# Performance work log

Measured on AMD Instinct MI355X. Metric: run time of the kernel, lower is better.

The kernel has to match this reference:

```python
import jax, jax.numpy as jnp
import numpy as np

NUM_HEADS = 16
HEAD_SIZE = 64
D_MODEL = NUM_HEADS * HEAD_SIZE  # 1024


def setup_inputs() -> dict:
    key = jax.random.key(0)
    ks = jax.random.split(key, 12)
    B, S = 4, 2048
    q = jax.random.normal(ks[0], (B, S, D_MODEL), dtype=jnp.float32)
    k = jax.random.normal(ks[1], (B, S, D_MODEL), dtype=jnp.float32)
    v = jax.random.normal(ks[2], (B, S, D_MODEL), dtype=jnp.float32)
    w = jax.random.uniform(ks[3], (B, S), dtype=jnp.float32)
    scale = 1.0 / np.sqrt(D_MODEL)
    Wq = jax.random.normal(ks[4], (D_MODEL, D_MODEL), dtype=jnp.float32) * scale
    Wk = jax.random.normal(ks[5], (D_MODEL, D_MODEL), dtype=jnp.float32) * scale
    Wv = jax.random.normal(ks[6], (D_MODEL, D_MODEL), dtype=jnp.float32) * scale
    Wo = jax.random.normal(ks[7], (D_MODEL, D_MODEL), dtype=jnp.float32) * scale
    bq = jnp.zeros((D_MODEL,), jnp.float32)
    bk = jnp.zeros((D_MODEL,), jnp.float32)
    bv = jnp.zeros((D_MODEL,), jnp.float32)
    bo = jnp.zeros((D_MODEL,), jnp.float32)
    return {"q": q, "k": k, "v": v, "w": w,
            "Wq": Wq, "bq": bq, "Wk": Wk, "bk": bk,
            "Wv": Wv, "bv": bv, "Wo": Wo, "bo": bo}


def reference(q, k, v, w, Wq, bq, Wk, bk, Wv, bv, Wo, bo):
    B, S, _ = q.shape
    H, Dh = NUM_HEADS, HEAD_SIZE

    def split_heads(x):  # [B,S,D] -> [B,H,S,Dh]
        return x.reshape(B, -1, H, Dh).transpose(0, 2, 1, 3)

    q_h = split_heads(q @ Wq + bq)
    k_h = split_heads(k @ Wk + bk)
    v_h = split_heads(v @ Wv + bv)

    # [B,H,Sq,Sk]
    score = jnp.einsum('bhqd,bhkd->bhqk', q_h, k_h) / jnp.sqrt(
        jnp.asarray(Dh, jnp.float32))
    # weighted unnormalized softmax: exp(score)*w / sum (no max subtraction,
    # faithful to original)
    exp_score = jnp.exp(score) * w[:, None, None, :]
    attn = exp_score / (jnp.sum(exp_score, axis=-1, keepdims=True) + 1e-12)

    context = jnp.einsum('bhqk,bhkd->bhqd', attn, v_h)  # [B,H,S,Dh]
    context = context.transpose(0, 2, 1, 3).reshape(B, -1, H * Dh)
    return context @ Wo + bo
```

## Files before the change

### kernel.cpp

```cpp
#include <hip/hip_runtime.h>
#include <hip/hip_bf16.h>

typedef __bf16 bf16x8 __attribute__((ext_vector_type(8)));
typedef float f32x4 __attribute__((ext_vector_type(4)));
typedef float f32x16 __attribute__((ext_vector_type(16)));
typedef unsigned short u16;
typedef unsigned int u32;

#define SB 4
#define SS 2048
#define SD 1024
#define SH 16
#define SDH 64

__device__ __forceinline__ u16 f2bf(float f) {
  union { float f; u32 u; } x; x.f = f;
  u32 r = (x.u + 0x7FFFu + ((x.u >> 16) & 1u)) >> 16;
  return (u16)r;
}

__device__ __forceinline__ void gl_lds16(const void* g, void* l) {
  __builtin_amdgcn_global_load_lds(
      (__attribute__((address_space(1))) void*)g,
      (__attribute__((address_space(3))) void*)l, 16, 0, 0);
}

__global__ void log2w_kernel(const float* __restrict__ w,
                             float* __restrict__ lwg) {
  int i = blockIdx.x * 256 + threadIdx.x;
  lwg[i] = __builtin_amdgcn_logf(w[i]);
}

__global__ void transpose_cast_kernel(const float* __restrict__ W0,
                                      const float* __restrict__ W1,
                                      const float* __restrict__ W2,
                                      const float* __restrict__ W3,
                                      u16* __restrict__ T0,
                                      u16* __restrict__ T1,
                                      u16* __restrict__ T2,
                                      u16* __restrict__ T3) {
  __shared__ float t[32][33];
  int z = blockIdx.z;
  const float* W = (z == 0) ? W0 : (z == 1) ? W1 : (z == 2) ? W2 : W3;
  u16* Wt = (z == 0) ? T0 : (z == 1) ? T1 : (z == 2) ? T2 : T3;
  int bx = blockIdx.x, by = blockIdx.y;
  int tx = threadIdx.x, ty = threadIdx.y;
#pragma unroll
  for (int j = 0; j < 32; j += 8)
    t[ty + j][tx] = W[(size_t)(by * 32 + ty + j) * SD + bx * 32 + tx];
  __syncthreads();
#pragma unroll
  for (int j = 0; j < 32; j += 8)
    Wt[(size_t)(bx * 32 + ty + j) * SD + by * 32 + tx] = f2bf(t[tx][ty + j]);
}

template <int MODE>
__global__ __launch_bounds__(256, 2)
void gemm_bt(const void* __restrict__ Ap, const void* __restrict__ Btp,
             const float* __restrict__ bias, void* __restrict__ Out,
             int M, int N, int K) {
  constexpr bool CA = (MODE == 0 || MODE == 1);
  constexpr bool CB = (MODE == 2);
  __shared__ u16 Asl[2][128 * 64];
  __shared__ u16 Bsl[2][128 * 64];
  const u16* Ab = (const u16*)Ap;
  const float* Af = (const float*)Ap;
  const u16* Bb = (const u16*)Btp;
  const float* Bf = (const float*)Btp;

  const int ntile = N >> 7;
  int bid = blockIdx.x;
  bid = (bid & 7) * ((int)gridDim.x >> 3) + (bid >> 3);
  int m0 = (bid / ntile) * 128, n0 = (bid % ntile) * 128;
  int tid = threadIdx.x;
  int lane = tid & 63, wv = tid >> 6;
  int wr = wv >> 1, wc = wv & 1;

  float4 regA[4][2], regB[4][2];

  auto load_cast = [&](int k0) {
#pragma unroll
    for (int it = 0; it < 4; ++it) {
      int c = tid + it * 256;
      int row = c >> 3, sl = c & 7;
      if (CA) {
        const float* s = Af + (size_t)(m0 + row) * K + k0 + sl * 8;
        regA[it][0] = *(const float4*)s;
        regA[it][1] = *(const float4*)(s + 4);
      }
      if (CB) {
        const float* s = Bf + (size_t)(n0 + row) * K + k0 + sl * 8;
        regB[it][0] = *(const float4*)s;
        regB[it][1] = *(const float4*)(s + 4);
      }
    }
  };
  auto stage_lds = [&](int buf, int k0) {
#pragma unroll
    for (int it = 0; it < 4; ++it) {
      int c = tid + it * 256;
      int row = c >> 3, sl = c & 7;
      int ssl = sl ^ (row & 7);
      if (!CA)
        gl_lds16(Ab + (size_t)(m0 + row) * K + k0 + ssl * 8,
                 (char*)&Asl[buf][0] + c * 16);
      if (!CB)
        gl_lds16(Bb + (size_t)(n0 + row) * K + k0 + ssl * 8,
                 (char*)&Bsl[buf][0] + c * 16);
    }
  };
  auto write_cast = [&](int buf) {
#pragma unroll
    for (int it = 0; it < 4; ++it) {
      int c = tid + it * 256;
      int row = c >> 3, sl = c & 7;
      int dst = (row * 128 + sl * 16) ^ ((row & 7) << 4);
      if (CA) {
        uint4 o;
        asm("v_cvt_pk_bf16_f32 %0, %1, %2"
            : "=v"(o.x) : "v"(regA[it][0].x), "v"(regA[it][0].y));
        asm("v_cvt_pk_bf16_f32 %0, %1, %2"
            : "=v"(o.y) : "v"(regA[it][0].z), "v"(regA[it][0].w));
        asm("v_cvt_pk_bf16_f32 %0, %1, %2"
            : "=v"(o.z) : "v"(regA[it][1].x), "v"(regA[it][1].y));
        asm("v_cvt_pk_bf16_f32 %0, %1, %2"
            : "=v"(o.w) : "v"(regA[it][1].z), "v"(regA[it][1].w));
        *(uint4*)((char*)&Asl[buf][0] + dst) = o;
      }
      if (CB) {
        uint4 o;
        asm("v_cvt_pk_bf16_f32 %0, %1, %2"
            : "=v"(o.x) : "v"(regB[it][0].x), "v"(regB[it][0].y));
        asm("v_cvt_pk_bf16_f32 %0, %1, %2"
            : "=v"(o.y) : "v"(regB[it][0].z), "v"(regB[it][0].w));
        asm("v_cvt_pk_bf16_f32 %0, %1, %2"
            : "=v"(o.z) : "v"(regB[it][1].x), "v"(regB[it][1].y));
        asm("v_cvt_pk_bf16_f32 %0, %1, %2"
            : "=v"(o.w) : "v"(regB[it][1].z), "v"(regB[it][1].w));
        *(uint4*)((char*)&Bsl[buf][0] + dst) = o;
      }
    }
  };

  f32x4 acc[4][4] = {};
  load_cast(0);
  stage_lds(0, 0);
  write_cast(0);

  int nk = K >> 6;
  for (int kt = 0; kt < nk; ++kt) {
    int buf = kt & 1;
    if (kt + 1 < nk) {
      load_cast((kt + 1) << 6);
      stage_lds(buf ^ 1, (kt + 1) << 6);
      if (CA || CB)
        asm volatile("s_waitcnt vmcnt(12) lgkmcnt(0)" ::: "memory");
      else
        asm volatile("s_waitcnt vmcnt(8) lgkmcnt(0)" ::: "memory");
    } else {
      asm volatile("s_waitcnt vmcnt(0) lgkmcnt(0)" ::: "memory");
    }
    __builtin_amdgcn_s_barrier();
#pragma unroll
    for (int kk = 0; kk < 2; ++kk) {
      bf16x8 af[4], bfr[4];
#pragma unroll
      for (int i = 0; i < 4; ++i) {
        int ar = wr * 64 + i * 16 + (lane & 15);
        int abyt = (ar * 128 + (kk * 32 + (lane >> 4) * 8) * 2) ^
                   ((ar & 7) << 4);
        af[i] = *(const bf16x8*)((const char*)&Asl[buf][0] + abyt);
        int br = wc * 64 + i * 16 + (lane & 15);
        int bbyt = (br * 128 + (kk * 32 + (lane >> 4) * 8) * 2) ^
                   ((br & 7) << 4);
        bfr[i] = *(const bf16x8*)((const char*)&Bsl[buf][0] + bbyt);
      }
#pragma unroll
      for (int i = 0; i < 4; ++i)
#pragma unroll
        for (int j = 0; j < 4; ++j)
          acc[i][j] = __builtin_amdgcn_mfma_f32_16x16x32_bf16(
              af[i], bfr[j], acc[i][j], 0, 0, 0);
    }
    if (kt + 1 < nk) write_cast(buf ^ 1);
    __builtin_amdgcn_s_barrier();
  }

  int cg = lane >> 4, cc = lane & 15;
#pragma unroll
  for (int i = 0; i < 4; ++i) {
#pragma unroll
    for (int j = 0; j < 4; ++j) {
#pragma unroll
      for (int r = 0; r < 4; ++r) {
        int m = m0 + wr * 64 + i * 16 + cg * 4 + r;
        int n = n0 + wc * 64 + j * 16 + cc;
        float val = acc[i][j][r];
        if (MODE == 0) {
          val = (val + bias[n]) * 0.18033688011112042f;
          int b = m >> 11, s = m & 2047, h = n >> 6, dh = n & 63;
          ((u16*)Out)[((size_t)((b * SH + h) * SS + s) << 6) + dh] = f2bf(val);
        } else if (MODE == 1) {
          val += bias[n];
          int b = m >> 11, s = m & 2047, h = n >> 6, dh = n & 63;
          size_t off = ((size_t)(b * SH + h) << 17) + ((size_t)(s >> 5) << 11) +
                       ((size_t)(dh >> 4) << 9) +
                       ((size_t)((s & 31) | ((dh & 8) << 2)) << 3) + (dh & 7);
          ((u16*)Out)[off] = f2bf(val);
        } else if (MODE == 2) {
          val += bias[m];
          int h = m >> 6, dh = m & 63, b = n >> 11, s = n & 2047;
          size_t off = ((size_t)(b * SH + h) << 17) + ((size_t)(s >> 4) << 10) +
                       ((size_t)(dh >> 5) << 9) +
                       ((size_t)(((s >> 3) & 1) * 32 + (dh & 31)) << 3) +
                       (s & 7);
          ((u16*)Out)[off] = f2bf(val);
        } else {
          val += bias[n];
          ((float*)Out)[(size_t)m * N + n] = val;
        }
      }
    }
  }
}

__global__ __launch_bounds__(256, 2)
void attn_kernel(const u16* __restrict__ Qh, const u16* __restrict__ Kf,
                 const u16* __restrict__ Vf, const float* __restrict__ lwg,
                 u16* __restrict__ Ctx) {
  __shared__ u16 Kl[3][4096];
  __shared__ u16 Vl[3][4096];

  int bid = blockIdx.x;
  int swz = (bid & 7) * 64 + (bid >> 3);
  int bh = swz >> 3;
  int qt = swz & 7;
  int b = bh >> 4, hh = bh & 15;
  int q0 = qt * 256;
  int tid = threadIdx.x, lane = tid & 63, wv = tid >> 6;
  int ql = lane & 31, h = lane >> 5;
  const size_t basebh = (size_t)bh * (SS * SDH);
  const char* Ksrc = (const char*)(Kf + basebh);
  const char* Vsrc = (const char*)(Vf + basebh);
  const float* lwp = lwg + b * SS;

  bf16x8 qf[2][4];
#pragma unroll
  for (int u = 0; u < 2; ++u) {
    const u16* qp =
        Qh + basebh + (size_t)(q0 + wv * 64 + u * 32 + ql) * SDH + h * 8;
#pragma unroll
    for (int st = 0; st < 4; ++st) qf[u][st] = *(const bf16x8*)(qp + st * 16);
  }

  auto stage = [&](int s, int t) {
#pragma unroll
    for (int it = 0; it < 2; ++it) {
      int c = tid + it * 256;
      gl_lds16(Ksrc + (size_t)t * 8192 + c * 16, (char*)&Kl[s][0] + c * 16);
      gl_lds16(Vsrc + (size_t)t * 8192 + c * 16, (char*)&Vl[s][0] + c * 16);
    }
  };

  f32x16 ctx[2][2] = {};
  float rs[2] = {0.f, 0.f};

  auto compute = [&](const char* Ks, const char* Vs, int t) {
    int kvb = t * 64;
    u32 pk[2][8][2];
#pragma unroll
    for (int kt = 0; kt < 2; ++kt) {
      bf16x8 kf[4];
#pragma unroll
      for (int st = 0; st < 4; ++st)
        kf[st] = *(const bf16x8*)(Ks + (kt * 4 + st) * 1024 + lane * 16);
      float4 lw[4];
#pragma unroll
      for (int e2 = 0; e2 < 4; ++e2)
        lw[e2] = *(const float4*)(lwp + kvb + kt * 32 + e2 * 8 + h * 4);
#pragma unroll
      for (int u = 0; u < 2; ++u) {
        f32x16 sc;
#pragma unroll
        for (int e2 = 0; e2 < 4; ++e2) {
          sc[e2 * 4 + 0] = lw[e2].x;
          sc[e2 * 4 + 1] = lw[e2].y;
          sc[e2 * 4 + 2] = lw[e2].z;
          sc[e2 * 4 + 3] = lw[e2].w;
        }
        __builtin_amdgcn_s_setprio(1);
#pragma unroll
        for (int st = 0; st < 4; ++st)
          sc = __builtin_amdgcn_mfma_f32_32x32x16_bf16(kf[st], qf[u][st], sc,
                                                       0, 0, 0);
        __builtin_amdgcn_s_setprio(0);
#pragma unroll
        for (int e2 = 0; e2 < 4; ++e2) {
          float v0 = __builtin_amdgcn_exp2f(sc[e2 * 4 + 0]);
          float v1 = __builtin_amdgcn_exp2f(sc[e2 * 4 + 1]);
          float v2 = __builtin_amdgcn_exp2f(sc[e2 * 4 + 2]);
          float v3 = __builtin_amdgcn_exp2f(sc[e2 * 4 + 3]);
          rs[u] += (v0 + v1) + (v2 + v3);
          u32 p0, p1;
          asm("v_cvt_pk_bf16_f32 %0, %1, %2" : "=v"(p0) : "v"(v0), "v"(v1));
          asm("v_cvt_pk_bf16_f32 %0, %1, %2" : "=v"(p1) : "v"(v2), "v"(v3));
          pk[u][kt * 4 + e2][0] = p0;
          pk[u][kt * 4 + e2][1] = p1;
        }
      }
    }
#pragma unroll
    for (int ksl = 0; ksl < 4; ++ksl) {
      bf16x8 vf0 = *(const bf16x8*)(Vs + (ksl * 2 + 0) * 1024 + lane * 16);
      bf16x8 vf1 = *(const bf16x8*)(Vs + (ksl * 2 + 1) * 1024 + lane * 16);
#pragma unroll
      for (int u = 0; u < 2; ++u) {
        u32 d0 = pk[u][2 * ksl][0], d1 = pk[u][2 * ksl][1];
        u32 s0 = pk[u][2 * ksl + 1][0], s1 = pk[u][2 * ksl + 1][1];
        asm("v_permlane32_swap_b32 %0, %1" : "+v"(d0), "+v"(s0));
        asm("v_permlane32_swap_b32 %0, %1" : "+v"(d1), "+v"(s1));
        union { u32 uu[4]; bf16x8 v; } pa;
        pa.uu[0] = d0; pa.uu[1] = d1; pa.uu[2] = s0; pa.uu[3] = s1;
        __builtin_amdgcn_s_setprio(1);
        ctx[u][0] = __builtin_amdgcn_mfma_f32_32x32x16_bf16(pa.v, vf0,
                                                            ctx[u][0], 0, 0, 0);
        ctx[u][1] = __builtin_amdgcn_mfma_f32_32x32x16_bf16(pa.v, vf1,
                                                            ctx[u][1], 0, 0, 0);
        __builtin_amdgcn_s_setprio(0);
      }
    }
  };

  stage(0, 0);
  stage(1, 1);

  for (int t = 0; t < 32; ++t) {
    if (t < 31)
      asm volatile("s_waitcnt vmcnt(4)" ::: "memory");
    else
      asm volatile("s_waitcnt vmcnt(0)" ::: "memory");
    __builtin_amdgcn_s_barrier();
    if (t + 2 < 32) stage((t + 2) % 3, t + 2);
    int s = t % 3;
    compute((const char*)&Kl[s][0], (const char*)&Vl[s][0], t);
  }

#pragma unroll
  for (int u = 0; u < 2; ++u) {
    float rsu = rs[u];
    rsu += __shfl_xor(rsu, 32, 64);
    float rinv = 1.0f / (rsu + 1e-12f);
#pragma unroll
    for (int reg = 0; reg < 16; ++reg) {
      int qrow = (reg & 3) + 8 * (reg >> 2) + 4 * h;
      float ri = __shfl(rinv, qrow, 64);
      int srow = q0 + wv * 64 + u * 32 + qrow;
      size_t base = ((size_t)(b * SS + srow) << 10) + hh * SDH;
      Ctx[base + ql] = f2bf(ctx[u][0][reg] * ri);
      Ctx[base + 32 + ql] = f2bf(ctx[u][1][reg] * ri);
    }
  }
}

extern "C" void kernel_launch(void* const* d_in, const int* in_sizes, int n_in,
                              void* d_out, int out_size, void* d_ws,
                              size_t ws_size, hipStream_t stream) {
  const float* q = (const float*)d_in[0];
  const float* k = (const float*)d_in[1];
  const float* v = (const float*)d_in[2];
  const float* w = (const float*)d_in[3];
  const float* Wq = (const float*)d_in[4];
  const float* bq = (const float*)d_in[5];
  const float* Wk = (const float*)d_in[6];
  const float* bk = (const float*)d_in[7];
  const float* Wv = (const float*)d_in[8];
  const float* bv = (const float*)d_in[9];
  const float* Wo = (const float*)d_in[10];
  const float* bo = (const float*)d_in[11];
  float* out = (float*)d_out;

  char* ws = (char*)d_ws;
  const size_t SZ = (size_t)8192 * 1024 * 2;
  u16* Ctx = (u16*)(ws);
  u16* WqT = (u16*)(ws + 3 * SZ);
  u16* WkT = WqT + 1024 * 1024;
  u16* WvT = WkT + 1024 * 1024;
  u16* WoT = WvT + 1024 * 1024;
  u16* Qh = (u16*)(ws + 3 * SZ + (size_t)4 * 1024 * 1024 * 2);
  u16* Kf = Qh + (size_t)8192 * 1024;
  u16* Vf = Kf + (size_t)8192 * 1024;
  float* lwg = (float*)(ws + 3 * SZ + (size_t)4 * 1024 * 1024 * 2 +
                        (size_t)3 * 8192 * 1024 * 2);

  log2w_kernel<<<32, 256, 0, stream>>>(w, lwg);
  dim3 tb(32, 8), tg(32, 32, 4);
  transpose_cast_kernel<<<tg, tb, 0, stream>>>(Wq, Wk, Wv, Wo,
                                               WqT, WkT, WvT, WoT);

  gemm_bt<0><<<512, 256, 0, stream>>>(q, WqT, bq, Qh, 8192, 1024, 1024);
  gemm_bt<1><<<512, 256, 0, stream>>>(k, WkT, bk, Kf, 8192, 1024, 1024);
  gemm_bt<2><<<512, 256, 0, stream>>>(WvT, v, bv, Vf, 1024, 8192, 1024);

  attn_kernel<<<512, 256, 0, stream>>>(Qh, Kf, Vf, lwg, Ctx);

  gemm_bt<3><<<512, 256, 0, stream>>>(Ctx, WoT, bo, out, 8192, 1024, 1024);
}
```

Baseline: 223.6 us.

## Pre-cast inputs to bf16 and software-pipeline QK/PV in attention

Adds standalone kernels that cast q, k and v to bf16 before the projection GEMMs. The GEMMs can then stage both operands with direct global-to-LDS loads instead of loading fp32 into registers and converting in-loop. Separately, the attention kernel moves from a 3-stage to a 4-stage LDS ring and splits compute into QK and PV phases. PV of the previous tile is interleaved with QK of the current one, using double-buffered packed probabilities. The cost is an extra full read and write of the inputs through the cast kernels, plus more LDS and registers in attention.

```diff
diff --git a/kernel.cpp b/kernel.cpp
--- a/kernel.cpp
+++ b/kernel.cpp
@@ -23,6 +23,20 @@
   __builtin_amdgcn_global_load_lds(
       (__attribute__((address_space(1))) void*)g,
       (__attribute__((address_space(3))) void*)l, 16, 0, 0);
+}
+
+__global__ void cast_bf16_kernel(const float* __restrict__ in,
+                                 u32* __restrict__ out, int n8) {
+  int i = blockIdx.x * blockDim.x + threadIdx.x;
+  if (i >= n8) return;
+  const float4* inp = (const float4*)in;
+  float4 a = inp[2 * i], b = inp[2 * i + 1];
+  uint4 o;
+  asm("v_cvt_pk_bf16_f32 %0, %1, %2" : "=v"(o.x) : "v"(a.x), "v"(a.y));
+  asm("v_cvt_pk_bf16_f32 %0, %1, %2" : "=v"(o.y) : "v"(a.z), "v"(a.w));
+  asm("v_cvt_pk_bf16_f32 %0, %1, %2" : "=v"(o.z) : "v"(b.x), "v"(b.y));
+  asm("v_cvt_pk_bf16_f32 %0, %1, %2" : "=v"(o.w) : "v"(b.z), "v"(b.w));
+  ((uint4*)out)[i] = o;
 }
 
 __global__ void log2w_kernel(const float* __restrict__ w,
@@ -56,18 +70,11 @@
 
 template <int MODE>
 __global__ __launch_bounds__(256, 2)
-void gemm_bt(const void* __restrict__ Ap, const void* __restrict__ Btp,
+void gemm_bt(const u16* __restrict__ A, const u16* __restrict__ Bt,
              const float* __restrict__ bias, void* __restrict__ Out,
              int M, int N, int K) {
-  constexpr bool CA = (MODE == 0 || MODE == 1);
-  constexpr bool CB = (MODE == 2);
   __shared__ u16 Asl[2][128 * 64];
   __shared__ u16 Bsl[2][128 * 64];
-  const u16* Ab = (const u16*)Ap;
-  const float* Af = (const float*)Ap;
-  const u16* Bb = (const u16*)Btp;
-  const float* Bf = (const float*)Btp;
-
   const int ntile = N >> 7;
   int bid = blockIdx.x;
   bid = (bid & 7) * ((int)gridDim.x >> 3) + (bid >> 3);
@@ -76,87 +83,28 @@
   int lane = tid & 63, wv = tid >> 6;
   int wr = wv >> 1, wc = wv & 1;
 
-  float4 regA[4][2], regB[4][2];
-
-  auto load_cast = [&](int k0) {
-#pragma unroll
-    for (int it = 0; it < 4; ++it) {
-      int c = tid + it * 256;
-      int row = c >> 3, sl = c & 7;
-      if (CA) {
-        const float* s = Af + (size_t)(m0 + row) * K + k0 + sl * 8;
-        regA[it][0] = *(const float4*)s;
-        regA[it][1] = *(const float4*)(s + 4);
-      }
-      if (CB) {
-        const float* s = Bf + (size_t)(n0 + row) * K + k0 + sl * 8;
-        regB[it][0] = *(const float4*)s;
-        regB[it][1] = *(const float4*)(s + 4);
-      }
-    }
-  };
-  auto stage_lds = [&](int buf, int k0) {
+  auto stage = [&](int buf, int k0) {
 #pragma unroll
     for (int it = 0; it < 4; ++it) {
       int c = tid + it * 256;
       int row = c >> 3, sl = c & 7;
       int ssl = sl ^ (row & 7);
-      if (!CA)
-        gl_lds16(Ab + (size_t)(m0 + row) * K + k0 + ssl * 8,
-                 (char*)&Asl[buf][0] + c * 16);
-      if (!CB)
-        gl_lds16(Bb + (size_t)(n0 + row) * K + k0 + ssl * 8,
-                 (char*)&Bsl[buf][0] + c * 16);
+      gl_lds16(A + (size_t)(m0 + row) * K + k0 + ssl * 8,
+               (char*)&Asl[buf][0] + c * 16);
+      gl_lds16(Bt + (size_t)(n0 + row) * K + k0 + ssl * 8,
+               (char*)&Bsl[buf][0] + c * 16);
     }
   };
-  auto write_cast = [&](int buf) {
-#pragma unroll
-    for (int it = 0; it < 4; ++it) {
-      int c = tid + it * 256;
-      int row = c >> 3, sl = c & 7;
-      int dst = (row * 128 + sl * 16) ^ ((row & 7) << 4);
-      if (CA) {
-        uint4 o;
-        asm("v_cvt_pk_bf16_f32 %0, %1, %2"
-            : "=v"(o.x) : "v"(regA[it][0].x), "v"(regA[it][0].y));
-        asm("v_cvt_pk_bf16_f32 %0, %1, %2"
-            : "=v"(o.y) : "v"(regA[it][0].z), "v"(regA[it][0].w));
-        asm("v_cvt_pk_bf16_f32 %0, %1, %2"
-            : "=v"(o.z) : "v"(regA[it][1].x), "v"(regA[it][1].y));
-        asm("v_cvt_pk_bf16_f32 %0, %1, %2"
-            : "=v"(o.w) : "v"(regA[it][1].z), "v"(regA[it][1].w));
-        *(uint4*)((char*)&Asl[buf][0] + dst) = o;
-      }
-      if (CB) {
-        uint4 o;
-        asm("v_cvt_pk_bf16_f32 %0, %1, %2"
-            : "=v"(o.x) : "v"(regB[it][0].x), "v"(regB[it][0].y));
-        asm("v_cvt_pk_bf16_f32 %0, %1, %2"
-            : "=v"(o.y) : "v"(regB[it][0].z), "v"(regB[it][0].w));
-        asm("v_cvt_pk_bf16_f32 %0, %1, %2"
-            : "=v"(o.z) : "v"(regB[it][1].x), "v"(regB[it][1].y));
-        asm("v_cvt_pk_bf16_f32 %0, %1, %2"
-            : "=v"(o.w) : "v"(regB[it][1].z), "v"(regB[it][1].w));
-        *(uint4*)((char*)&Bsl[buf][0] + dst) = o;
-      }
-    }
-  };
 
   f32x4 acc[4][4] = {};
-  load_cast(0);
-  stage_lds(0, 0);
-  write_cast(0);
+  stage(0, 0);
 
   int nk = K >> 6;
   for (int kt = 0; kt < nk; ++kt) {
     int buf = kt & 1;
     if (kt + 1 < nk) {
-      load_cast((kt + 1) << 6);
-      stage_lds(buf ^ 1, (kt + 1) << 6);
-      if (CA || CB)
-        asm volatile("s_waitcnt vmcnt(12) lgkmcnt(0)" ::: "memory");
-      else
-        asm volatile("s_waitcnt vmcnt(8) lgkmcnt(0)" ::: "memory");
+      stage(buf ^ 1, (kt + 1) << 6);
+      asm volatile("s_waitcnt vmcnt(8) lgkmcnt(0)" ::: "memory");
     } else {
       asm volatile("s_waitcnt vmcnt(0) lgkmcnt(0)" ::: "memory");
     }
@@ -182,7 +130,6 @@
           acc[i][j] = __builtin_amdgcn_mfma_f32_16x16x32_bf16(
               af[i], bfr[j], acc[i][j], 0, 0, 0);
     }
-    if (kt + 1 < nk) write_cast(buf ^ 1);
     __builtin_amdgcn_s_barrier();
   }
 
@@ -228,8 +175,8 @@
 void attn_kernel(const u16* __restrict__ Qh, const u16* __restrict__ Kf,
                  const u16* __restrict__ Vf, const float* __restrict__ lwg,
                  u16* __restrict__ Ctx) {
-  __shared__ u16 Kl[3][4096];
-  __shared__ u16 Vl[3][4096];
+  __shared__ u16 Kl[4][4096];
+  __shared__ u16 Vl[4][4096];
 
   int bid = blockIdx.x;
   int swz = (bid & 7) * 64 + (bid >> 3);
@@ -264,10 +211,11 @@
 
   f32x16 ctx[2][2] = {};
   float rs[2] = {0.f, 0.f};
-
-  auto compute = [&](const char* Ks, const char* Vs, int t) {
+  u32 pkA[2][8][2], pkB[2][8][2];
+
+  auto qk = [&](int t, u32 (&pk)[2][8][2]) {
+    const char* Ks = (const char*)&Kl[t & 3][0];
     int kvb = t * 64;
-    u32 pk[2][8][2];
 #pragma unroll
     for (int kt = 0; kt < 2; ++kt) {
       bf16x8 kf[4];
@@ -309,6 +257,10 @@
         }
       }
     }
+  };
+
+  auto pv = [&](int t, u32 (&pk)[2][8][2]) {
+    const char* Vs = (const char*)&Vl[t & 3][0];
 #pragma unroll
     for (int ksl = 0; ksl < 4; ++ksl) {
       bf16x8 vf0 = *(const bf16x8*)(Vs + (ksl * 2 + 0) * 1024 + lane * 16);
@@ -334,16 +286,30 @@
   stage(0, 0);
   stage(1, 1);
 
-  for (int t = 0; t < 32; ++t) {
-    if (t < 31)
-      asm volatile("s_waitcnt vmcnt(4)" ::: "memory");
-    else
-      asm volatile("s_waitcnt vmcnt(0)" ::: "memory");
+  asm volatile("s_waitcnt vmcnt(4)" ::: "memory");
+  __builtin_amdgcn_s_barrier();
+  stage(2, 2);
+  qk(0, pkA);
+
+  for (int t = 1; t < 30; t += 2) {
+    asm volatile("s_waitcnt vmcnt(4)" ::: "memory");
     __builtin_amdgcn_s_barrier();
-    if (t + 2 < 32) stage((t + 2) % 3, t + 2);
-    int s = t % 3;
-    compute((const char*)&Kl[s][0], (const char*)&Vl[s][0], t);
-  }
+    stage((t + 2) & 3, t + 2);
+    pv(t - 1, pkA);
+    qk(t, pkB);
+
+    asm volatile("s_waitcnt vmcnt(4)" ::: "memory");
+    __builtin_amdgcn_s_barrier();
+    if (t + 3 < 32) stage((t + 3) & 3, t + 3);
+    pv(t, pkB);
+    qk(t + 1, pkA);
+  }
+
+  asm volatile("s_waitcnt vmcnt(0)" ::: "memory");
+  __builtin_amdgcn_s_barrier();
+  pv(30, pkA);
+  qk(31, pkB);
+  pv(31, pkB);
 
 #pragma unroll
   for (int u = 0; u < 2; ++u) {
@@ -381,7 +347,9 @@
 
   char* ws = (char*)d_ws;
   const size_t SZ = (size_t)8192 * 1024 * 2;
-  u16* Ctx = (u16*)(ws);
+  u16* qb = (u16*)(ws);
+  u16* kb = (u16*)(ws + SZ);
+  u16* vb = (u16*)(ws + 2 * SZ);
   u16* WqT = (u16*)(ws + 3 * SZ);
   u16* WkT = WqT + 1024 * 1024;
   u16* WvT = WkT + 1024 * 1024;
@@ -391,15 +359,19 @@
   u16* Vf = Kf + (size_t)8192 * 1024;
   float* lwg = (float*)(ws + 3 * SZ + (size_t)4 * 1024 * 1024 * 2 +
                         (size_t)3 * 8192 * 1024 * 2);
-
+  u16* Ctx = qb;
+
+  cast_bf16_kernel<<<4096, 256, 0, stream>>>(q, (u32*)qb, 1048576);
+  cast_bf16_kernel<<<4096, 256, 0, stream>>>(k, (u32*)kb, 1048576);
+  cast_bf16_kernel<<<4096, 256, 0, stream>>>(v, (u32*)vb, 1048576);
   log2w_kernel<<<32, 256, 0, stream>>>(w, lwg);
   dim3 tb(32, 8), tg(32, 32, 4);
   transpose_cast_kernel<<<tg, tb, 0, stream>>>(Wq, Wk, Wv, Wo,
                                                WqT, WkT, WvT, WoT);
 
-  gemm_bt<0><<<512, 256, 0, stream>>>(q, WqT, bq, Qh, 8192, 1024, 1024);
-  gemm_bt<1><<<512, 256, 0, stream>>>(k, WkT, bk, Kf, 8192, 1024, 1024);
-  gemm_bt<2><<<512, 256, 0, stream>>>(WvT, v, bv, Vf, 1024, 8192, 1024);
+  gemm_bt<0><<<512, 256, 0, stream>>>(qb, WqT, bq, Qh, 8192, 1024, 1024);
+  gemm_bt<1><<<512, 256, 0, stream>>>(kb, WkT, bk, Kf, 8192, 1024, 1024);
+  gemm_bt<2><<<512, 256, 0, stream>>>(WvT, vb, bv, Vf, 1024, 8192, 1024);
 
   attn_kernel<<<512, 256, 0, stream>>>(Qh, Kf, Vf, lwg, Ctx);
 
```

Result: faster. 210.2 us (-6.0%).
